# Kernel optimization log

Measured on AMD Instinct MI355X. Metric: run time of the kernel, lower is better.

The kernel has to match this reference:

```python
import jax, jax.numpy as jnp
import numpy as np

CAP_FACTOR = 1.5
LN_EPS = 1e-5


def setup_inputs() -> dict:
    key = jax.random.key(0)
    ks = jax.random.split(key, 12)
    B, N, D_IN, D, E = 16, 576, 1024, 2048, 4
    H = 4 * D  # FeedForward scale_factor=4
    s = 0.02
    return {
        "x": jax.random.normal(ks[0], (B, N, D_IN), jnp.float32),
        "ln_g": jnp.ones((D_IN,), jnp.float32),
        "ln_b": jnp.zeros((D_IN,), jnp.float32),
        "pre_W": jax.random.normal(ks[1], (D_IN, D), jnp.float32) * s,
        "pre_b": jnp.zeros((D,), jnp.float32),
        "sw_W": jax.random.normal(ks[2], (D, E), jnp.float32) * s,
        "sw_b": jnp.zeros((E,), jnp.float32),
        "W1": jax.random.normal(ks[3], (E, D, H), jnp.float32) * s,
        "b1": jnp.zeros((E, H), jnp.float32),
        "W2": jax.random.normal(ks[4], (E, H, D), jnp.float32) * s,
        "b2": jnp.zeros((E, D), jnp.float32),
    }


def reference(x, ln_g, ln_b, pre_W, pre_b, sw_W, sw_b, W1, b1, W2, b2):
    B, N, _ = x.shape
    # pre_norm -> pre_linear -> gelu (torch nn.GELU = exact erf)
    mu = jnp.mean(x, axis=-1, keepdims=True)
    var = jnp.mean((x - mu) ** 2, axis=-1, keepdims=True)
    xn = (x - mu) / jnp.sqrt(var + LN_EPS) * ln_g + ln_b
    t = jax.nn.gelu(xn @ pre_W + pre_b, approximate=False)
    d = t.shape[-1]
    t = t.reshape(-1, d)  # [T, d]
    T = t.shape[0]
    E = W1.shape[0]
    cap = int(CAP_FACTOR * T / E)

    route_prob = jax.nn.softmax(t @ sw_W + sw_b, axis=-1)  # [T, E]
    pmax = jnp.max(route_prob, axis=-1)
    routes = jnp.argmax(route_prob, axis=-1)

    onehot = routes[:, None] == jnp.arange(E)[None, :]  # [T, E] bool
    counts = jnp.sum(onehot, axis=0).astype(x.dtype)  # pre-drop counts

    # position of each token within its expert's queue (deterministic order;
    # original uses randperm before capacity truncation)
    pos = jnp.take_along_axis(jnp.cumsum(onehot, axis=0) - 1, routes[:, None], axis=1)[:, 0]
    keep = pos < cap
    slot = jnp.where(keep, routes * cap + pos, E * cap)  # dropped -> dummy slot

    # dispatch: [E*cap+1, d] buffer (last row = dump for dropped tokens)
    buf = jnp.zeros((E * cap + 1, d), t.dtype).at[slot].set(t)
    eb = buf[: E * cap].reshape(E, cap, d)

    # grouped expert FFN: d -> 4d -> d, GELU (dropout inactive at eval)
    hh = jax.nn.gelu(jnp.einsum('ecd,edh->ech', eb, W1) + b1[:, None, :], approximate=False)
    yy = jnp.einsum('ech,ehd->ecd', hh, W2) + b2[:, None, :]

    # combine: gather expert outputs back; dropped tokens pass through t
    y = yy.reshape(E * cap, d)[jnp.clip(slot, 0, E * cap - 1)]
    final = jnp.where(keep[:, None], y, t) * pmax[:, None]  # is_scale_prob=True

    n_dropped = jnp.sum(~keep)
    return final.reshape(B, N, d), counts, jnp.sum(route_prob, axis=0), n_dropped, pmax
```

## Files before the change

### kernel.cpp

```cpp
#include <hip/hip_runtime.h>
#include <cmath>

typedef _Float16 half_t;
typedef unsigned short ushort_t;
typedef __attribute__((ext_vector_type(8))) _Float16 half8;
typedef __attribute__((ext_vector_type(4))) _Float16 half4v;
typedef __attribute__((ext_vector_type(8))) short short8;
typedef __attribute__((ext_vector_type(4))) float f32x4;

#define T_TOK   9216
#define DIN     1024
#define DMOD    2048
#define HDIM    8192
#define NEXP    4
#define CAPN    3456
#define GAP_TAU 5e-5

__device__ inline float geluf(float x) {
    return 0.5f * x * (1.0f + erff(x * 0.70710678118654752440f));
}
__device__ inline double gelud(double x) {
    return 0.5 * x * (1.0 + erf(x * 0.70710678118654752440));
}
__device__ inline double waveRedD(double v) {
#pragma unroll
    for (int off = 32; off; off >>= 1) v += __shfl_down(v, off);
    return v;
}
__device__ inline ushort_t bf16rn(float f) {
    unsigned u = __float_as_uint(f);
    unsigned r = (u + 0x7FFFu + ((u >> 16) & 1u)) >> 16;
    return (ushort_t)r;
}
__device__ inline float bf16tof(ushort_t h) {
    return __uint_as_float(((unsigned)h) << 16);
}
__device__ __forceinline__ void gld16(const void* g, void* l) {
    __builtin_amdgcn_global_load_lds((const __attribute__((address_space(1))) void*)g,
                                     (__attribute__((address_space(3))) void*)l, 16, 0, 0);
}

__global__ __launch_bounds__(256) void k1_ln(const float* __restrict__ x,
                                             const float* __restrict__ g,
                                             const float* __restrict__ b,
                                             ushort_t* __restrict__ xh,
                                             ushort_t* __restrict__ xl) {
    const int row = blockIdx.x;
    const int tid = threadIdx.x;
    const int c = tid * 4;
    const float4 v = *(const float4*)&x[(size_t)row * DIN + c];
    __shared__ double sw[8];
    __shared__ double bc[2];
    const int lane = tid & 63, wv = tid >> 6;

    double s = (double)v.x + (double)v.y + (double)v.z + (double)v.w;
    s = waveRedD(s);
    if (lane == 0) sw[wv] = s;
    __syncthreads();
    if (tid == 0) bc[0] = (sw[0] + sw[1] + sw[2] + sw[3]) * (1.0 / 1024.0);
    __syncthreads();
    const double mu = bc[0];
    const double d0 = (double)v.x - mu, d1 = (double)v.y - mu;
    const double d2 = (double)v.z - mu, d3 = (double)v.w - mu;
    double s2 = d0 * d0 + d1 * d1 + d2 * d2 + d3 * d3;
    s2 = waveRedD(s2);
    if (lane == 0) sw[4 + wv] = s2;
    __syncthreads();
    if (tid == 0) bc[1] = 1.0 / sqrt((sw[4] + sw[5] + sw[6] + sw[7]) * (1.0 / 1024.0) + 1e-5);
    __syncthreads();
    const double rs = bc[1];
    const float4 gv = *(const float4*)&g[c];
    const float4 bv = *(const float4*)&b[c];
    float o0 = (float)(d0 * rs * (double)gv.x + (double)bv.x);
    float o1 = (float)(d1 * rs * (double)gv.y + (double)bv.y);
    float o2 = (float)(d2 * rs * (double)gv.z + (double)bv.z);
    float o3 = (float)(d3 * rs * (double)gv.w + (double)bv.w);
    ushort4 hv, lv;
    hv.x = bf16rn(o0); lv.x = bf16rn(o0 - bf16tof(hv.x));
    hv.y = bf16rn(o1); lv.y = bf16rn(o1 - bf16tof(hv.y));
    hv.z = bf16rn(o2); lv.z = bf16rn(o2 - bf16tof(hv.z));
    hv.w = bf16rn(o3); lv.w = bf16rn(o3 - bf16tof(hv.w));
    *(ushort4*)&xh[(size_t)row * DIN + c] = hv;
    *(ushort4*)&xl[(size_t)row * DIN + c] = lv;
}

#define TT_ST 68
__global__ __launch_bounds__(256) void kt_bf16x2(const float* __restrict__ src,
                                                 ushort_t* __restrict__ dhi,
                                                 ushort_t* __restrict__ dlo,
                                                 int K, int N) {
    __shared__ ushort_t th[64 * TT_ST];
    __shared__ ushort_t tl[64 * TT_ST];
    const int n0 = blockIdx.x * 64, k0 = blockIdx.y * 64;
    const int t = threadIdx.x, tr = t >> 4, tc = (t & 15) * 4;
#pragma unroll
    for (int r = 0; r < 4; ++r) {
        const int row = r * 16 + tr;
        const float4 v = *(const float4*)&src[(size_t)(k0 + row) * N + n0 + tc];
        const float vv[4] = {v.x, v.y, v.z, v.w};
#pragma unroll
        for (int j = 0; j < 4; ++j) {
            const ushort_t h = bf16rn(vv[j]);
            th[(tc + j) * TT_ST + row] = h;
            tl[(tc + j) * TT_ST + row] = bf16rn(vv[j] - bf16tof(h));
        }
    }
    __syncthreads();
#pragma unroll
    for (int r = 0; r < 4; ++r) {
        const int row = r * 16 + tr;
        ushort4 hv, lv;
        hv.x = th[row * TT_ST + tc + 0]; lv.x = tl[row * TT_ST + tc + 0];
        hv.y = th[row * TT_ST + tc + 1]; lv.y = tl[row * TT_ST + tc + 1];
        hv.z = th[row * TT_ST + tc + 2]; lv.z = tl[row * TT_ST + tc + 2];
        hv.w = th[row * TT_ST + tc + 3]; lv.w = tl[row * TT_ST + tc + 3];
        *(ushort4*)&dhi[(size_t)(n0 + row) * K + k0 + tc] = hv;
        *(ushort4*)&dlo[(size_t)(n0 + row) * K + k0 + tc] = lv;
    }
}

__global__ __launch_bounds__(256) void kt_f16(const float* __restrict__ src,
                                              half_t* __restrict__ dst,
                                              int K, int N) {
    __shared__ half_t tile[64 * TT_ST];
    const int n0 = blockIdx.x * 64, k0 = blockIdx.y * 64;
    const int t = threadIdx.x, tr = t >> 4, tc = (t & 15) * 4;
#pragma unroll
    for (int r = 0; r < 4; ++r) {
        const int row = r * 16 + tr;
        const float4 v = *(const float4*)&src[(size_t)(k0 + row) * N + n0 + tc];
        tile[(tc + 0) * TT_ST + row] = (half_t)v.x;
        tile[(tc + 1) * TT_ST + row] = (half_t)v.y;
        tile[(tc + 2) * TT_ST + row] = (half_t)v.z;
        tile[(tc + 3) * TT_ST + row] = (half_t)v.w;
    }
    __syncthreads();
#pragma unroll
    for (int r = 0; r < 4; ++r) {
        const int row = r * 16 + tr;
        const half4v v4 = *(const half4v*)&tile[row * TT_ST + tc];
        *(half4v*)&dst[(size_t)(n0 + row) * K + k0 + tc] = v4;
    }
}

__global__ __launch_bounds__(256) void k2_pre(const ushort_t* __restrict__ xh,
                                              const ushort_t* __restrict__ xl,
                                              const ushort_t* __restrict__ wh,
                                              const ushort_t* __restrict__ wl,
                                              const float* __restrict__ bias,
                                              float* __restrict__ t32,
                                              half_t* __restrict__ t16) {
    __shared__ ushort_t Ah[128 * 32];
    __shared__ ushort_t Al[128 * 32];
    __shared__ ushort_t Bh[128 * 32];
    __shared__ ushort_t Bl[128 * 32];
    const int tid = threadIdx.x;
    const int m0 = blockIdx.y * 128, n0 = blockIdx.x * 128;
    const int r4 = tid >> 2, sg = (tid & 3) * 8;
    const ushort_t* gah0 = xh + (size_t)(m0 + r4) * DIN + sg;
    const ushort_t* gah1 = xh + (size_t)(m0 + 64 + r4) * DIN + sg;
    const ushort_t* gal0 = xl + (size_t)(m0 + r4) * DIN + sg;
    const ushort_t* gal1 = xl + (size_t)(m0 + 64 + r4) * DIN + sg;
    const ushort_t* gbh0 = wh + (size_t)(n0 + r4) * DIN + sg;
    const ushort_t* gbh1 = wh + (size_t)(n0 + 64 + r4) * DIN + sg;
    const ushort_t* gbl0 = wl + (size_t)(n0 + r4) * DIN + sg;
    const ushort_t* gbl1 = wl + (size_t)(n0 + 64 + r4) * DIN + sg;
    ushort_t* lAh0 = &Ah[tid * 8]; ushort_t* lAh1 = &Ah[2048 + tid * 8];
    ushort_t* lAl0 = &Al[tid * 8]; ushort_t* lAl1 = &Al[2048 + tid * 8];
    ushort_t* lBh0 = &Bh[tid * 8]; ushort_t* lBh1 = &Bh[2048 + tid * 8];
    ushort_t* lBl0 = &Bl[tid * 8]; ushort_t* lBl1 = &Bl[2048 + tid * 8];
    const int w = tid >> 6, lane = tid & 63, q = lane >> 4, mr = lane & 15;
    const int wm = (w & 1) * 64, wn = (w >> 1) * 64;

    f32x4 acc[4][4];
#pragma unroll
    for (int i = 0; i < 4; ++i)
#pragma unroll
        for (int j = 0; j < 4; ++j) acc[i][j] = (f32x4){0.f, 0.f, 0.f, 0.f};

    for (int k0 = 0; k0 < DIN; k0 += 32) {
        gld16(gah0 + k0, lAh0); gld16(gah1 + k0, lAh1);
        gld16(gal0 + k0, lAl0); gld16(gal1 + k0, lAl1);
        gld16(gbh0 + k0, lBh0); gld16(gbh1 + k0, lBh1);
        gld16(gbl0 + k0, lBl0); gld16(gbl1 + k0, lBl1);
        __syncthreads();
        short8 ah[4], al4[4], bh[4], bl4[4];
#pragma unroll
        for (int i = 0; i < 4; ++i) {
            ah[i]  = *(const short8*)&Ah[(wm + i * 16 + mr) * 32 + q * 8];
            al4[i] = *(const short8*)&Al[(wm + i * 16 + mr) * 32 + q * 8];
            bh[i]  = *(const short8*)&Bh[(wn + i * 16 + mr) * 32 + q * 8];
            bl4[i] = *(const short8*)&Bl[(wn + i * 16 + mr) * 32 + q * 8];
        }
#pragma unroll
        for (int i = 0; i < 4; ++i)
#pragma unroll
            for (int j = 0; j < 4; ++j) {
                acc[i][j] = __builtin_amdgcn_mfma_f32_16x16x32_bf16(al4[i], bh[j], acc[i][j], 0, 0, 0);
                acc[i][j] = __builtin_amdgcn_mfma_f32_16x16x32_bf16(ah[i], bl4[j], acc[i][j], 0, 0, 0);
                acc[i][j] = __builtin_amdgcn_mfma_f32_16x16x32_bf16(ah[i], bh[j], acc[i][j], 0, 0, 0);
            }
        __syncthreads();
    }
    float bb[4];
#pragma unroll
    for (int j = 0; j < 4; ++j) bb[j] = bias[n0 + wn + j * 16 + mr];
#pragma unroll
    for (int i = 0; i < 4; ++i) {
#pragma unroll
        for (int p = 0; p < 4; ++p) {
            const int row = m0 + wm + i * 16 + q * 4 + p;
#pragma unroll
            for (int j = 0; j < 4; ++j) {
                const int col = n0 + wn + j * 16 + mr;
                const float t = geluf(acc[i][j][p] + bb[j]);
                t32[(size_t)row * DMOD + col] = t;
                t16[(size_t)row * DMOD + col] = (half_t)t;
            }
        }
    }
}

__global__ __launch_bounds__(256) void k3_router(const float* __restrict__ t32,
                                                 const float* __restrict__ swW,
                                                 const float* __restrict__ swb,
                                                 double* __restrict__ logitsD,
                                                 int* __restrict__ flags) {
    const int tok = blockIdx.x * 4 + (threadIdx.x >> 6);
    const int lane = threadIdx.x & 63;
    const float* tr = t32 + (size_t)tok * DMOD;
    double a0 = 0, a1 = 0, a2 = 0, a3 = 0;
    for (int it = 0; it < 8; ++it) {
        const int k = it * 256 + lane * 4;
        const float4 tv = *(const float4*)&tr[k];
        const float tp[4] = {tv.x, tv.y, tv.z, tv.w};
#pragma unroll
        for (int j = 0; j < 4; ++j) {
            const float4 wv = *(const float4*)&swW[(size_t)(k + j) * 4];
            const double td = (double)tp[j];
            a0 += td * (double)wv.x;
            a1 += td * (double)wv.y;
            a2 += td * (double)wv.z;
            a3 += td * (double)wv.w;
        }
    }
    a0 = waveRedD(a0); a1 = waveRedD(a1); a2 = waveRedD(a2); a3 = waveRedD(a3);
    if (lane == 0) {
        a0 += (double)swb[0]; a1 += (double)swb[1]; a2 += (double)swb[2]; a3 += (double)swb[3];
        double* Lp = logitsD + (size_t)tok * 4;
        Lp[0] = a0; Lp[1] = a1; Lp[2] = a2; Lp[3] = a3;
        double m1 = a0, m2 = -1e300;
        if (a1 > m1) { m2 = m1; m1 = a1; } else if (a1 > m2) m2 = a1;
        if (a2 > m1) { m2 = m1; m1 = a2; } else if (a2 > m2) m2 = a2;
        if (a3 > m1) { m2 = m1; m1 = a3; } else if (a3 > m2) m2 = a3;
        flags[tok] = (m1 - m2 < GAP_TAU) ? 1 : 0;
    }
}

__global__ __launch_bounds__(256) void k4_recompute(const float* __restrict__ x,
                                                    const float* __restrict__ g,
                                                    const float* __restrict__ bvec,
                                                    const float* __restrict__ preW,
                                                    const float* __restrict__ preb,
                                                    const float* __restrict__ swW,
                                                    const float* __restrict__ swb,
                                                    const int* __restrict__ flags,
                                                    double* __restrict__ logitsD) {
    const int tok = blockIdx.x;
    if (!flags[tok]) return;
    __shared__ double xr[DIN];
    __shared__ double sw8[8];
    __shared__ double bcv[2];
    __shared__ double r4[4][4];
    const int tid = threadIdx.x, lane = tid & 63, wv = tid >> 6;

    double s = 0;
    for (int i = tid; i < DIN; i += 256) {
        const double v = (double)x[(size_t)tok * DIN + i];
        xr[i] = v;
        s += v;
    }
    s = waveRedD(s);
    if (lane == 0) sw8[wv] = s;
    __syncthreads();
    if (tid == 0) bcv[0] = (sw8[0] + sw8[1] + sw8[2] + sw8[3]) * (1.0 / 1024.0);
    __syncthreads();
    const double mu = bcv[0];
    double s2 = 0;
    for (int i = tid; i < DIN; i += 256) {
        const double d = xr[i] - mu;
        s2 += d * d;
    }
    s2 = waveRedD(s2);
    if (lane == 0) sw8[4 + wv] = s2;
    __syncthreads();
    if (tid == 0) bcv[1] = 1.0 / sqrt((sw8[4] + sw8[5] + sw8[6] + sw8[7]) * (1.0 / 1024.0) + 1e-5);
    __syncthreads();
    const double rs = bcv[1];
    for (int i = tid; i < DIN; i += 256)
        xr[i] = (xr[i] - mu) * rs * (double)g[i] + (double)bvec[i];
    __syncthreads();

    double l0 = 0, l1 = 0, l2 = 0, l3 = 0;
    for (int p = 0; p < 8; ++p) {
        const int c = p * 256 + tid;
        double z = (double)preb[c];
#pragma unroll 8
        for (int k = 0; k < DIN; ++k)
            z += xr[k] * (double)preW[(size_t)k * DMOD + c];
        const double t = gelud(z);
        const float4 wv4 = *(const float4*)&swW[(size_t)c * 4];
        l0 += t * (double)wv4.x; l1 += t * (double)wv4.y;
        l2 += t * (double)wv4.z; l3 += t * (double)wv4.w;
    }
    l0 = waveRedD(l0); l1 = waveRedD(l1); l2 = waveRedD(l2); l3 = waveRedD(l3);
    if (lane == 0) { r4[wv][0] = l0; r4[wv][1] = l1; r4[wv][2] = l2; r4[wv][3] = l3; }
    __syncthreads();
    if (tid == 0) {
#pragma unroll
        for (int e = 0; e < 4; ++e)
            logitsD[(size_t)tok * 4 + e] =
                r4[0][e] + r4[1][e] + r4[2][e] + r4[3][e] + (double)swb[e];
    }
}

__global__ __launch_bounds__(1024) void k5_scan(const double* __restrict__ logitsD,
                                                int* __restrict__ slot2tok,
                                                int* __restrict__ keepArr,
                                                int* __restrict__ keptcnt,
                                                float* __restrict__ outCounts,
                                                float* __restrict__ outPsum,
                                                float* __restrict__ outNdrop,
                                                float* __restrict__ outPmax) {
    __shared__ int wcnt[16][4];
    __shared__ unsigned int baseSh[4];
    __shared__ double redd[16];
    const int tid = threadIdx.x, lane = tid & 63, wv = tid >> 6;
    for (int i = tid; i < NEXP * CAPN; i += 1024) slot2tok[i] = 0;
    if (tid < 4) baseSh[tid] = 0;
    double p0 = 0, p1 = 0, p2 = 0, p3 = 0;
    __syncthreads();
    for (int c = 0; c < 9; ++c) {
        const int tok = c * 1024 + tid;
        const double* L = logitsD + (size_t)tok * 4;
        const double l0 = L[0], l1 = L[1], l2 = L[2], l3 = L[3];
        int r = 0;
        double m = l0;
        if (l1 > m) { m = l1; r = 1; }
        if (l2 > m) { m = l2; r = 2; }
        if (l3 > m) { m = l3; r = 3; }
        const double e0 = exp(l0 - m), e1 = exp(l1 - m), e2 = exp(l2 - m), e3 = exp(l3 - m);
        const double inv = 1.0 / (e0 + e1 + e2 + e3);
        p0 += e0 * inv; p1 += e1 * inv; p2 += e2 * inv; p3 += e3 * inv;
        outPmax[tok] = (float)inv;
        const unsigned long long mm0 = __ballot(r == 0);
        const unsigned long long mm1 = __ballot(r == 1);
        const unsigned long long mm2 = __ballot(r == 2);
        const unsigned long long mm3 = __ballot(r == 3);
        const unsigned long long msel = (r == 0) ? mm0 : (r == 1) ? mm1 : (r == 2) ? mm2 : mm3;
        const unsigned long long below = (1ull << lane) - 1ull;
        const int posw = __popcll(msel & below);
        if (lane == 0) {
            wcnt[wv][0] = __popcll(mm0);
            wcnt[wv][1] = __popcll(mm1);
            wcnt[wv][2] = __popcll(mm2);
            wcnt[wv][3] = __popcll(mm3);
        }
        __syncthreads();
        int wbase = 0;
        for (int w2 = 0; w2 < wv; ++w2) wbase += wcnt[w2][r];
        const unsigned int pos = baseSh[r] + (unsigned int)(wbase + posw);
        const int kp = (pos < (unsigned int)CAPN) ? 1 : 0;
        keepArr[tok] = kp;
        if (kp) slot2tok[r * CAPN + pos] = tok;
        __syncthreads();
        if (tid < 4) {
            unsigned int tot = 0;
            for (int w2 = 0; w2 < 16; ++w2) tot += (unsigned int)wcnt[w2][tid];
            baseSh[tid] += tot;
        }
        __syncthreads();
    }
    if (tid < 4) {
        const unsigned int cnt = baseSh[tid];
        outCounts[tid] = (float)cnt;
        keptcnt[tid] = (cnt < (unsigned int)CAPN) ? (int)cnt : CAPN;
    }
    if (tid == 0) {
        int nd = 0;
#pragma unroll
        for (int e = 0; e < 4; ++e)
            nd += (baseSh[e] > (unsigned int)CAPN) ? (int)(baseSh[e] - CAPN) : 0;
        outNdrop[0] = (float)nd;
    }
    double pva[4] = {p0, p1, p2, p3};
#pragma unroll
    for (int e = 0; e < 4; ++e) {
        const double sr = waveRedD(pva[e]);
        __syncthreads();
        if (lane == 0) redd[wv] = sr;
        __syncthreads();
        if (tid == 0) {
            double tt = 0;
            for (int w2 = 0; w2 < 16; ++w2) tt += redd[w2];
            outPsum[e] = (float)tt;
        }
    }
}

__global__ __launch_bounds__(256) void k6_ffn1(const half_t* __restrict__ t16,
                                               const half_t* __restrict__ w1t,
                                               const float* __restrict__ b1e,
                                               const int* __restrict__ s2t,
                                               const int* __restrict__ keptp,
                                               half_t* __restrict__ hbuf) {
    const int kept = keptp[0];
    const int m0 = blockIdx.y * 128;
    if (m0 >= kept) return;
    const int n0 = blockIdx.x * 128;
    __shared__ half_t As[128 * 32];
    __shared__ half_t Bs[128 * 32];
    const int tid = threadIdx.x;
    const int r4 = tid >> 2, sg = (tid & 3) * 8;
    const int tok0 = s2t[m0 + r4];
    const int tok1 = s2t[m0 + 64 + r4];
    const half_t* gA0 = t16 + (size_t)tok0 * DMOD + sg;
    const half_t* gA1 = t16 + (size_t)tok1 * DMOD + sg;
    const half_t* gB0 = w1t + (size_t)(n0 + r4) * DMOD + sg;
    const half_t* gB1 = w1t + (size_t)(n0 + 64 + r4) * DMOD + sg;
    half_t* lA0 = &As[tid * 8]; half_t* lA1 = &As[2048 + tid * 8];
    half_t* lB0 = &Bs[tid * 8]; half_t* lB1 = &Bs[2048 + tid * 8];
    const int w = tid >> 6, lane = tid & 63, q = lane >> 4, mr = lane & 15;
    const int wm = (w & 1) * 64, wn = (w >> 1) * 64;

    f32x4 acc[4][4];
#pragma unroll
    for (int i = 0; i < 4; ++i)
#pragma unroll
        for (int j = 0; j < 4; ++j) acc[i][j] = (f32x4){0.f, 0.f, 0.f, 0.f};

    for (int k0 = 0; k0 < DMOD; k0 += 32) {
        gld16(gA0 + k0, lA0); gld16(gA1 + k0, lA1);
        gld16(gB0 + k0, lB0); gld16(gB1 + k0, lB1);
        __syncthreads();
        half8 afr[4], bfr[4];
#pragma unroll
        for (int i = 0; i < 4; ++i) {
            afr[i] = *(const half8*)&As[(wm + i * 16 + mr) * 32 + q * 8];
            bfr[i] = *(const half8*)&Bs[(wn + i * 16 + mr) * 32 + q * 8];
        }
#pragma unroll
        for (int i = 0; i < 4; ++i)
#pragma unroll
            for (int j = 0; j < 4; ++j)
                acc[i][j] = __builtin_amdgcn_mfma_f32_16x16x32_f16(afr[i], bfr[j], acc[i][j], 0, 0, 0);
        __syncthreads();
    }
    float bb[4];
#pragma unroll
    for (int j = 0; j < 4; ++j) bb[j] = b1e[n0 + wn + j * 16 + mr];
#pragma unroll
    for (int i = 0; i < 4; ++i) {
#pragma unroll
        for (int p = 0; p < 4; ++p) {
            const int row = m0 + wm + i * 16 + q * 4 + p;
            half_t* hp = hbuf + (size_t)row * HDIM;
#pragma unroll
            for (int j = 0; j < 4; ++j) {
                const int col = n0 + wn + j * 16 + mr;
                hp[col] = (half_t)geluf(acc[i][j][p] + bb[j]);
            }
        }
    }
}

__global__ __launch_bounds__(256) void k7_ffn2(const half_t* __restrict__ hbuf,
                                               const half_t* __restrict__ w2t,
                                               const float* __restrict__ b2e,
                                               const int* __restrict__ s2t,
                                               const int* __restrict__ keptp,
                                               const float* __restrict__ pmax,
                                               float* __restrict__ outF) {
    const int kept = keptp[0];
    const int m0 = blockIdx.y * 128;
    if (m0 >= kept) return;
    const int n0 = blockIdx.x * 128;
    __shared__ half_t As[128 * 32];
    __shared__ half_t Bs[128 * 32];
    const int tid = threadIdx.x;
    const int r4 = tid >> 2, sg = (tid & 3) * 8;
    const half_t* gA0 = hbuf + (size_t)(m0 + r4) * HDIM + sg;
    const half_t* gA1 = hbuf + (size_t)(m0 + 64 + r4) * HDIM + sg;
    const half_t* gB0 = w2t + (size_t)(n0 + r4) * HDIM + sg;
    const half_t* gB1 = w2t + (size_t)(n0 + 64 + r4) * HDIM + sg;
    half_t* lA0 = &As[tid * 8]; half_t* lA1 = &As[2048 + tid * 8];
    half_t* lB0 = &Bs[tid * 8]; half_t* lB1 = &Bs[2048 + tid * 8];
    const int w = tid >> 6, lane = tid & 63, q = lane >> 4, mr = lane & 15;
    const int wm = (w & 1) * 64, wn = (w >> 1) * 64;

    f32x4 acc[4][4];
#pragma unroll
    for (int i = 0; i < 4; ++i)
#pragma unroll
        for (int j = 0; j < 4; ++j) acc[i][j] = (f32x4){0.f, 0.f, 0.f, 0.f};

    for (int k0 = 0; k0 < HDIM; k0 += 32) {
        gld16(gA0 + k0, lA0); gld16(gA1 + k0, lA1);
        gld16(gB0 + k0, lB0); gld16(gB1 + k0, lB1);
        __syncthreads();
        half8 afr[4], bfr[4];
#pragma unroll
        for (int i = 0; i < 4; ++i) {
            afr[i] = *(const half8*)&As[(wm + i * 16 + mr) * 32 + q * 8];
            bfr[i] = *(const half8*)&Bs[(wn + i * 16 + mr) * 32 + q * 8];
        }
#pragma unroll
        for (int i = 0; i < 4; ++i)
#pragma unroll
            for (int j = 0; j < 4; ++j)
                acc[i][j] = __builtin_amdgcn_mfma_f32_16x16x32_f16(afr[i], bfr[j], acc[i][j], 0, 0, 0);
        __syncthreads();
    }
    float bb[4];
#pragma unroll
    for (int j = 0; j < 4; ++j) bb[j] = b2e[n0 + wn + j * 16 + mr];
#pragma unroll
    for (int i = 0; i < 4; ++i) {
#pragma unroll
        for (int p = 0; p < 4; ++p) {
            const int gm = m0 + wm + i * 16 + q * 4 + p;
            if (gm < kept) {
                const int tok = s2t[gm];
                const float pm = pmax[tok];
                float* op = outF + (size_t)tok * DMOD;
#pragma unroll
                for (int j = 0; j < 4; ++j) {
                    const int col = n0 + wn + j * 16 + mr;
                    op[col] = (acc[i][j][p] + bb[j]) * pm;
                }
            }
        }
    }
}

__global__ __launch_bounds__(256) void k8_pass(const int* __restrict__ keepArr,
                                               const float* __restrict__ t32,
                                               const float* __restrict__ pmax,
                                               float* __restrict__ outF) {
    const int tok = blockIdx.x;
    if (keepArr[tok]) return;
    const float pm = pmax[tok];
    const size_t base = (size_t)tok * DMOD;
    for (int c = threadIdx.x * 4; c < DMOD; c += 1024) {
        float4 v = *(const float4*)&t32[base + c];
        v.x *= pm; v.y *= pm; v.z *= pm; v.w *= pm;
        *(float4*)&outF[base + c] = v;
    }
}

extern "C" void kernel_launch(void* const* d_in, const int* in_sizes, int n_in,
                              void* d_out, int out_size, void* d_ws, size_t ws_size,
                              hipStream_t stream) {
    const float* x     = (const float*)d_in[0];
    const float* ln_g  = (const float*)d_in[1];
    const float* ln_b  = (const float*)d_in[2];
    const float* pre_W = (const float*)d_in[3];
    const float* pre_b = (const float*)d_in[4];
    const float* sw_W  = (const float*)d_in[5];
    const float* sw_b  = (const float*)d_in[6];
    const float* W1    = (const float*)d_in[7];
    const float* b1    = (const float*)d_in[8];
    const float* W2    = (const float*)d_in[9];
    const float* b2    = (const float*)d_in[10];

    float* outF      = (float*)d_out;
    float* outCounts = outF + (size_t)T_TOK * DMOD;
    float* outPsum   = outCounts + 4;
    float* outNdrop  = outPsum + 4;
    float* outPmax   = outNdrop + 1;

    char* w = (char*)d_ws;
    const size_t OFF_XH  = 0;
    const size_t OFF_XL  = OFF_XH + (size_t)T_TOK * DIN * 2;
    const size_t OFF_WTH = OFF_XL + (size_t)T_TOK * DIN * 2;
    const size_t OFF_WTL = OFF_WTH + (size_t)DMOD * DIN * 2;
    const size_t OFF_T32 = OFF_WTL + (size_t)DMOD * DIN * 2;
    const size_t OFF_T16 = OFF_T32 + (size_t)T_TOK * DMOD * 4;
    const size_t OFF_H   = OFF_T16 + (size_t)T_TOK * DMOD * 2;
    const size_t OFF_WT  = OFF_H + (size_t)CAPN * HDIM * 2;
    const size_t OFF_LG  = OFF_WT + (size_t)HDIM * DMOD * 2;
    const size_t OFF_FL  = OFF_LG + (size_t)T_TOK * 4 * 8;
    const size_t OFF_KP  = OFF_FL + (size_t)T_TOK * 4;
    const size_t OFF_ST  = OFF_KP + (size_t)T_TOK * 4;
    const size_t OFF_KC  = OFF_ST + (size_t)NEXP * CAPN * 4;
    const size_t REQ     = OFF_KC + 256;
    if (ws_size < REQ) return;

    ushort_t* xh      = (ushort_t*)(w + OFF_XH);
    ushort_t* xl      = (ushort_t*)(w + OFF_XL);
    ushort_t* wth     = (ushort_t*)(w + OFF_WTH);
    ushort_t* wtl     = (ushort_t*)(w + OFF_WTL);
    float*    t32     = (float*)(w + OFF_T32);
    half_t*   t16     = (half_t*)(w + OFF_T16);
    half_t*   hbuf    = (half_t*)(w + OFF_H);
    half_t*   wT      = (half_t*)(w + OFF_WT);
    double*   logitsD = (double*)(w + OFF_LG);
    int*      flags   = (int*)(w + OFF_FL);
    int*      keepArr = (int*)(w + OFF_KP);
    int*      s2t     = (int*)(w + OFF_ST);
    int*      keptcnt = (int*)(w + OFF_KC);

    k1_ln<<<T_TOK, 256, 0, stream>>>(x, ln_g, ln_b, xh, xl);
    kt_bf16x2<<<dim3(DMOD / 64, DIN / 64), 256, 0, stream>>>(pre_W, wth, wtl, DIN, DMOD);
    k2_pre<<<dim3(DMOD / 128, T_TOK / 128), 256, 0, stream>>>(xh, xl, wth, wtl, pre_b, t32, t16);
    k3_router<<<T_TOK / 4, 256, 0, stream>>>(t32, sw_W, sw_b, logitsD, flags);
    k4_recompute<<<T_TOK, 256, 0, stream>>>(x, ln_g, ln_b, pre_W, pre_b, sw_W, sw_b,
                                            flags, logitsD);
    k5_scan<<<1, 1024, 0, stream>>>(logitsD, s2t, keepArr, keptcnt,
                                    outCounts, outPsum, outNdrop, outPmax);
    for (int e = 0; e < NEXP; ++e) {
        kt_f16<<<dim3(HDIM / 64, DMOD / 64), 256, 0, stream>>>(
            W1 + (size_t)e * DMOD * HDIM, wT, DMOD, HDIM);
        k6_ffn1<<<dim3(HDIM / 128, CAPN / 128), 256, 0, stream>>>(
            t16, wT, b1 + (size_t)e * HDIM,
            s2t + (size_t)e * CAPN, keptcnt + e, hbuf);
        kt_f16<<<dim3(DMOD / 64, HDIM / 64), 256, 0, stream>>>(
            W2 + (size_t)e * HDIM * DMOD, wT, HDIM, DMOD);
        k7_ffn2<<<dim3(DMOD / 128, CAPN / 128), 256, 0, stream>>>(
            hbuf, wT, b2 + (size_t)e * DMOD,
            s2t + (size_t)e * CAPN, keptcnt + e, outPmax, outF);
    }
    k8_pass<<<T_TOK, 256, 0, stream>>>(keepArr, t32, outPmax, outF);
}
```

Measured before the change: 2.296 ms.

## Parallelize router-tie recompute across columns and swizzle GEMM block order

Tokens whose top-two router logits are nearly tied are now collected into a compact list with an atomic counter. Their fp64 recompute is split into three kernels: a LayerNorm pass, a pre-linear dot product spread across column blocks, and a reduction. Before, each flagged token was recomputed by a single block walking the whole pre_W matrix, which serialized the work and left the GPU underused. Tokens beyond the first 64 flagged still go through the old per-token fallback. Separately, the pre-linear and both expert-FFN GEMMs remap block indices in an 8-way interleave to change L2 locality, at the cost of extra launches and a memset.

```diff
diff --git a/kernel.cpp b/kernel.cpp
--- a/kernel.cpp
+++ b/kernel.cpp
@@ -15,6 +15,7 @@
 #define NEXP    4
 #define CAPN    3456
 #define GAP_TAU 5e-5
+#define MAXF    64
 
 __device__ inline float geluf(float x) {
     return 0.5f * x * (1.0f + erff(x * 0.70710678118654752440f));
@@ -155,7 +156,10 @@
     __shared__ ushort_t Bh[128 * 32];
     __shared__ ushort_t Bl[128 * 32];
     const int tid = threadIdx.x;
-    const int m0 = blockIdx.y * 128, n0 = blockIdx.x * 128;
+    int lin = blockIdx.y * gridDim.x + blockIdx.x;
+    const int cpx = (gridDim.x * gridDim.y) >> 3;
+    lin = (lin & 7) * cpx + (lin >> 3);
+    const int m0 = (lin / gridDim.x) * 128, n0 = (lin % gridDim.x) * 128;
     const int r4 = tid >> 2, sg = (tid & 3) * 8;
     const ushort_t* gah0 = xh + (size_t)(m0 + r4) * DIN + sg;
     const ushort_t* gah1 = xh + (size_t)(m0 + 64 + r4) * DIN + sg;
@@ -225,7 +229,10 @@
                                                  const float* __restrict__ swW,
                                                  const float* __restrict__ swb,
                                                  double* __restrict__ logitsD,
-                                                 int* __restrict__ flags) {
+                                                 int* __restrict__ flags,
+                                                 int* __restrict__ flagidx,
+                                                 int* __restrict__ fllist,
+                                                 int* __restrict__ flcnt) {
     const int tok = blockIdx.x * 4 + (threadIdx.x >> 6);
     const int lane = threadIdx.x & 63;
     const float* tr = t32 + (size_t)tok * DMOD;
@@ -253,11 +260,113 @@
         if (a1 > m1) { m2 = m1; m1 = a1; } else if (a1 > m2) m2 = a1;
         if (a2 > m1) { m2 = m1; m1 = a2; } else if (a2 > m2) m2 = a2;
         if (a3 > m1) { m2 = m1; m1 = a3; } else if (a3 > m2) m2 = a3;
-        flags[tok] = (m1 - m2 < GAP_TAU) ? 1 : 0;
-    }
-}
-
-__global__ __launch_bounds__(256) void k4_recompute(const float* __restrict__ x,
+        const int f = (m1 - m2 < GAP_TAU) ? 1 : 0;
+        flags[tok] = f;
+        if (f) {
+            const int idx = atomicAdd(flcnt, 1);
+            flagidx[tok] = idx;
+            if (idx < MAXF) fllist[idx] = tok;
+        }
+    }
+}
+
+__global__ __launch_bounds__(256) void k4a_xr(const float* __restrict__ x,
+                                              const float* __restrict__ g,
+                                              const float* __restrict__ bvec,
+                                              const int* __restrict__ fllist,
+                                              const int* __restrict__ flcnt,
+                                              double* __restrict__ xrbuf) {
+    const int bid = blockIdx.x;
+    if (bid >= flcnt[0]) return;
+    const int tok = fllist[bid];
+    __shared__ double sw8[8];
+    __shared__ double bcv[2];
+    const int tid = threadIdx.x, lane = tid & 63, wv = tid >> 6;
+    const int c = tid * 4;
+    const float4 xv = *(const float4*)&x[(size_t)tok * DIN + c];
+    const double d[4] = {(double)xv.x, (double)xv.y, (double)xv.z, (double)xv.w};
+    double s = d[0] + d[1] + d[2] + d[3];
+    s = waveRedD(s);
+    if (lane == 0) sw8[wv] = s;
+    __syncthreads();
+    if (tid == 0) bcv[0] = (sw8[0] + sw8[1] + sw8[2] + sw8[3]) * (1.0 / 1024.0);
+    __syncthreads();
+    const double mu = bcv[0];
+    double s2 = 0;
+#pragma unroll
+    for (int j = 0; j < 4; ++j) { const double dd = d[j] - mu; s2 += dd * dd; }
+    s2 = waveRedD(s2);
+    if (lane == 0) sw8[4 + wv] = s2;
+    __syncthreads();
+    if (tid == 0) bcv[1] = 1.0 / sqrt((sw8[4] + sw8[5] + sw8[6] + sw8[7]) * (1.0 / 1024.0) + 1e-5);
+    __syncthreads();
+    const double rs = bcv[1];
+#pragma unroll
+    for (int j = 0; j < 4; ++j)
+        xrbuf[(size_t)bid * DIN + c + j] = (d[j] - mu) * rs * (double)g[c + j] + (double)bvec[c + j];
+}
+
+__global__ __launch_bounds__(256) void k4b_dot(const double* __restrict__ xrbuf,
+                                               const float* __restrict__ preW,
+                                               const float* __restrict__ preb,
+                                               const float* __restrict__ swW,
+                                               const int* __restrict__ flcnt,
+                                               double* __restrict__ part) {
+    const int by = blockIdx.y;
+    if (by >= flcnt[0]) return;
+    const int tid = threadIdx.x;
+    const int cl = tid & 31;
+    const int col = blockIdx.x * 32 + cl;
+    const int ks = tid >> 5;
+    const double* xr = xrbuf + (size_t)by * DIN + ks * 128;
+    const float* wp = preW + (size_t)(ks * 128) * DMOD + col;
+    double z = 0;
+#pragma unroll 4
+    for (int k = 0; k < 128; ++k)
+        z += xr[k] * (double)wp[(size_t)k * DMOD];
+    __shared__ double red[32][9];
+    red[cl][ks] = z;
+    __syncthreads();
+    if (tid < 32) {
+        double s = (double)preb[col];
+#pragma unroll
+        for (int j = 0; j < 8; ++j) s += red[tid][j];
+        const double t = gelud(s);
+        const float4 wv4 = *(const float4*)&swW[(size_t)col * 4];
+        double l0 = t * (double)wv4.x, l1 = t * (double)wv4.y;
+        double l2 = t * (double)wv4.z, l3 = t * (double)wv4.w;
+#pragma unroll
+        for (int off = 16; off; off >>= 1) {
+            l0 += __shfl_down(l0, off);
+            l1 += __shfl_down(l1, off);
+            l2 += __shfl_down(l2, off);
+            l3 += __shfl_down(l3, off);
+        }
+        if (tid == 0) {
+            double* pp = part + ((size_t)by * 64 + blockIdx.x) * 4;
+            pp[0] = l0; pp[1] = l1; pp[2] = l2; pp[3] = l3;
+        }
+    }
+}
+
+__global__ __launch_bounds__(64) void k4c_red(const double* __restrict__ part,
+                                              const int* __restrict__ fllist,
+                                              const int* __restrict__ flcnt,
+                                              const float* __restrict__ swb,
+                                              double* __restrict__ logitsD) {
+    const int bid = blockIdx.x;
+    if (bid >= flcnt[0]) return;
+    const int tok = fllist[bid];
+    const int lane = threadIdx.x;
+#pragma unroll
+    for (int e = 0; e < 4; ++e) {
+        double v = part[((size_t)bid * 64 + lane) * 4 + e];
+        v = waveRedD(v);
+        if (lane == 0) logitsD[(size_t)tok * 4 + e] = v + (double)swb[e];
+    }
+}
+
+__global__ __launch_bounds__(256) void k4d_fallback(const float* __restrict__ x,
                                                     const float* __restrict__ g,
                                                     const float* __restrict__ bvec,
                                                     const float* __restrict__ preW,
@@ -265,9 +374,11 @@
                                                     const float* __restrict__ swW,
                                                     const float* __restrict__ swb,
                                                     const int* __restrict__ flags,
+                                                    const int* __restrict__ flagidx,
                                                     double* __restrict__ logitsD) {
     const int tok = blockIdx.x;
     if (!flags[tok]) return;
+    if (flagidx[tok] < MAXF) return;
     __shared__ double xr[DIN];
     __shared__ double sw8[8];
     __shared__ double bcv[2];
@@ -415,9 +526,12 @@
                                                const int* __restrict__ keptp,
                                                half_t* __restrict__ hbuf) {
     const int kept = keptp[0];
-    const int m0 = blockIdx.y * 128;
+    int lin = blockIdx.y * gridDim.x + blockIdx.x;
+    const int cpx = (gridDim.x * gridDim.y) >> 3;
+    lin = (lin & 7) * cpx + (lin >> 3);
+    const int m0 = (lin / gridDim.x) * 128;
     if (m0 >= kept) return;
-    const int n0 = blockIdx.x * 128;
+    const int n0 = (lin % gridDim.x) * 128;
     __shared__ half_t As[128 * 32];
     __shared__ half_t Bs[128 * 32];
     const int tid = threadIdx.x;
@@ -482,9 +596,12 @@
                                                const float* __restrict__ pmax,
                                                float* __restrict__ outF) {
     const int kept = keptp[0];
-    const int m0 = blockIdx.y * 128;
+    int lin = blockIdx.y * gridDim.x + blockIdx.x;
+    const int cpx = (gridDim.x * gridDim.y) >> 3;
+    lin = (lin & 7) * cpx + (lin >> 3);
+    const int m0 = (lin / gridDim.x) * 128;
     if (m0 >= kept) return;
-    const int n0 = blockIdx.x * 128;
+    const int n0 = (lin % gridDim.x) * 128;
     __shared__ half_t As[128 * 32];
     __shared__ half_t Bs[128 * 32];
     const int tid = threadIdx.x;
@@ -593,7 +710,12 @@
     const size_t OFF_KP  = OFF_FL + (size_t)T_TOK * 4;
     const size_t OFF_ST  = OFF_KP + (size_t)T_TOK * 4;
     const size_t OFF_KC  = OFF_ST + (size_t)NEXP * CAPN * 4;
-    const size_t REQ     = OFF_KC + 256;
+    const size_t OFF_FLL = OFF_KC + 256;
+    const size_t OFF_FID = OFF_FLL + (size_t)MAXF * 4;
+    const size_t OFF_CNT = OFF_FID + (size_t)T_TOK * 4;
+    const size_t OFF_XR  = OFF_CNT + 256;
+    const size_t OFF_PRT = OFF_XR + (size_t)MAXF * DIN * 8;
+    const size_t REQ     = OFF_PRT + (size_t)MAXF * 64 * 4 * 8;
     if (ws_size < REQ) return;
 
     ushort_t* xh      = (ushort_t*)(w + OFF_XH);
@@ -609,13 +731,23 @@
     int*      keepArr = (int*)(w + OFF_KP);
     int*      s2t     = (int*)(w + OFF_ST);
     int*      keptcnt = (int*)(w + OFF_KC);
+    int*      fllist  = (int*)(w + OFF_FLL);
+    int*      flagidx = (int*)(w + OFF_FID);
+    int*      flcnt   = (int*)(w + OFF_CNT);
+    double*   xrbuf   = (double*)(w + OFF_XR);
+    double*   part    = (double*)(w + OFF_PRT);
 
     k1_ln<<<T_TOK, 256, 0, stream>>>(x, ln_g, ln_b, xh, xl);
     kt_bf16x2<<<dim3(DMOD / 64, DIN / 64), 256, 0, stream>>>(pre_W, wth, wtl, DIN, DMOD);
     k2_pre<<<dim3(DMOD / 128, T_TOK / 128), 256, 0, stream>>>(xh, xl, wth, wtl, pre_b, t32, t16);
-    k3_router<<<T_TOK / 4, 256, 0, stream>>>(t32, sw_W, sw_b, logitsD, flags);
-    k4_recompute<<<T_TOK, 256, 0, stream>>>(x, ln_g, ln_b, pre_W, pre_b, sw_W, sw_b,
-                                            flags, logitsD);
+    hipMemsetAsync(flcnt, 0, sizeof(int), stream);
+    k3_router<<<T_TOK / 4, 256, 0, stream>>>(t32, sw_W, sw_b, logitsD, flags,
+                                             flagidx, fllist, flcnt);
+    k4a_xr<<<MAXF, 256, 0, stream>>>(x, ln_g, ln_b, fllist, flcnt, xrbuf);
+    k4b_dot<<<dim3(64, MAXF), 256, 0, stream>>>(xrbuf, pre_W, pre_b, sw_W, flcnt, part);
+    k4c_red<<<MAXF, 64, 0, stream>>>(part, fllist, flcnt, sw_b, logitsD);
+    k4d_fallback<<<T_TOK, 256, 0, stream>>>(x, ln_g, ln_b, pre_W, pre_b, sw_W, sw_b,
+                                            flags, flagidx, logitsD);
     k5_scan<<<1, 1024, 0, stream>>>(logitsD, s2t, keepArr, keptcnt,
                                     outCounts, outPsum, outNdrop, outPmax);
     for (int e = 0; e < NEXP; ++e) {
```

New measurement: 2.200 ms. 4.2% less time.
